# Optimization experiments

Hardware: AMD Instinct MI355X
Metric: run time of the kernel (lower is better)

## Reference

```python
import jax, jax.numpy as jnp
import numpy as np

N = 200000   # total atoms in batched graph
E = 3200000  # total bonds (directed edges)
B = 512      # number of graphs / sequences
L = 1000     # miRNA sequence length


def _gcn(x, W, b, src, dst, dis):
    # PyG GCNConv: add self-loops, symmetric normalization D^-1/2 A D^-1/2
    h = x @ W                                   # [N, Fout]
    msg = (dis[src] * dis[dst])[:, None] * h[src]
    agg = jax.ops.segment_sum(msg, dst, num_segments=x.shape[0])
    return agg + (dis * dis)[:, None] * h + b   # self-loop term + bias


def _conv1d(x, k, b):
    # x: [B, C, L], k: [O, I, K]  (torch Conv1d, VALID padding)
    y = jax.lax.conv_general_dilated(x, k, (1,), 'VALID',
                                     dimension_numbers=('NCH', 'OIH', 'NCH'))
    return y + b[None, :, None]


def _mp3(x):
    # torch MaxPool1d(3): window 3, stride 3, floor
    return jax.lax.reduce_window(x, -jnp.inf, jax.lax.max, (1, 1, 3), (1, 1, 3), 'VALID')


def setup_inputs() -> dict:
    key = jax.random.key(0)
    ks = jax.random.split(key, 24)
    w = lambda k, s: (jax.random.normal(k, s, jnp.float32) * 0.1)
    p = {}
    p['x'] = jax.random.normal(ks[0], (N, 4), jnp.float32)
    p['edge_index'] = jax.random.randint(ks[1], (2, E), 0, N, jnp.int32)
    p['batch'] = (jnp.arange(N, dtype=jnp.int32) * B // N).astype(jnp.int32)  # every graph non-empty
    p['target'] = jax.random.normal(ks[2], (B, L, 5), jnp.float32)
    # GCN layers 4->4->8->16
    p['W1'] = w(ks[3], (4, 4));    p['b1'] = jnp.zeros(4, jnp.float32)
    p['W2'] = w(ks[4], (4, 8));    p['b2'] = jnp.zeros(8, jnp.float32)
    p['W3'] = w(ks[5], (8, 16));   p['b3'] = jnp.zeros(16, jnp.float32)
    p['Wg1'] = w(ks[6], (16, 1024)); p['bg1'] = jnp.zeros(1024, jnp.float32)
    p['Wg2'] = w(ks[7], (1024, 128)); p['bg2'] = jnp.zeros(128, jnp.float32)
    # CNN stack on sequences, kernels [O, I, 8]
    p['K1'] = w(ks[8], (32, 5, 8));   p['cb1'] = jnp.zeros(32, jnp.float32)
    p['K2'] = w(ks[9], (64, 32, 8));  p['cb2'] = jnp.zeros(64, jnp.float32)
    p['K3'] = w(ks[10], (128, 64, 8)); p['cb3'] = jnp.zeros(128, jnp.float32)
    p['Wxt'] = w(ks[11], (128, 128)); p['bxt'] = jnp.zeros(128, jnp.float32)
    # fusion head
    p['Wf1'] = w(ks[12], (256, 1024)); p['bf1'] = jnp.zeros(1024, jnp.float32)
    p['Wf2'] = w(ks[13], (1024, 512)); p['bf2'] = jnp.zeros(512, jnp.float32)
    p['Wo'] = w(ks[14], (512, 2));     p['bo'] = jnp.zeros(2, jnp.float32)
    return p


def reference(x, edge_index, batch, target, W1, b1, W2, b2, W3, b3,
              Wg1, bg1, Wg2, bg2, K1, cb1, K2, cb2, K3, cb3,
              Wxt, bxt, Wf1, bf1, Wf2, bf2, Wo, bo):
    src, dst = edge_index[0], edge_index[1]
    deg = jax.ops.segment_sum(jnp.ones(src.shape[0], x.dtype), dst,
                              num_segments=x.shape[0]) + 1.0  # +1 self-loop
    dis = jax.lax.rsqrt(deg)
    # Graph branch (dropout is identity in eval)
    h = jax.nn.relu(_gcn(x, W1, b1, src, dst, dis))
    h = jax.nn.relu(_gcn(h, W2, b2, src, dst, dis))
    h = jax.nn.relu(_gcn(h, W3, b3, src, dst, dis))
    g = jax.ops.segment_max(h, batch, num_segments=B)  # global_max_pool
    g = jax.nn.relu(g @ Wg1 + bg1)
    g = g @ Wg2 + bg2
    # Sequence branch
    t = jnp.transpose(target, (0, 2, 1))  # [B, 5, L]
    c = _mp3(jax.nn.relu(_conv1d(t, K1, cb1)))
    c = _mp3(jax.nn.relu(_conv1d(c, K2, cb2)))
    c = _mp3(jax.nn.relu(_conv1d(c, K3, cb3)))
    c = jnp.mean(c, axis=2)               # [B, 128]
    c = jax.nn.relu(c @ Wxt + bxt)
    # Fusion head
    xc = jnp.concatenate([g, c], axis=1)  # [B, 256]
    xc = jax.nn.relu(xc @ Wf1 + bf1)
    xc = jax.nn.relu(xc @ Wf2 + bf2)
    return xc @ Wo + bo                    # [B, 2]
```

## Files before the change

kernel.cpp:

```cpp
#include <hip/hip_runtime.h>
#include <hip/hip_fp16.h>
#include <cstddef>

#define NA 200000
#define NE 3200000
#define NB 512
#define NBKT 256
#define BKTN 782
#define BKTCAP 16384
#define NEPB 3200

typedef _Float16 hv2 __attribute__((ext_vector_type(2)));
typedef _Float16 half8 __attribute__((ext_vector_type(8)));
typedef float floatx4 __attribute__((ext_vector_type(4)));
union UH2 { unsigned u; __half2 h; hv2 v; };
__device__ __forceinline__ float4 h4f(unsigned a, unsigned b) {
    UH2 x, y; x.u = a; y.u = b;
    float2 fa = __half22float2(x.h), fb = __half22float2(y.h);
    return make_float4(fa.x, fa.y, fb.x, fb.y);
}
__device__ __forceinline__ unsigned f2h(float a, float b) {
    UH2 r; r.h = __float22half2_rn(make_float2(a, b));
    return r.u;
}

__global__ void k_init(unsigned* g, int* gcursor,
                       float* gvec, const float* __restrict__ bg2,
                       float* xf2, const float* __restrict__ bf2,
                       float* xf1, const float* __restrict__ bf1,
                       const float* __restrict__ K2, const float* __restrict__ K3,
                       __half* __restrict__ Wt2, __half* __restrict__ Wt3) {
    int i = blockIdx.x * blockDim.x + threadIdx.x;
    if (i < NB * 16) g[i] = 0u;
    if (i < NBKT) gcursor[i] = i * BKTCAP;
    if (i < NB * 128) gvec[i] = bg2[i & 127];
    if (i < NB * 512) xf2[i] = bf2[i & 511];
    if (i < NB * 1024) xf1[i] = bf1[i & 1023];
    if (i < 64 * 32 * 8) {
        int o = i >> 8, rem = i & 255, c = rem >> 3, kk = rem & 7;
        Wt2[(o << 8) + (kk << 5) + c] = __float2half(K2[i]);
    }
    if (i < 128 * 64 * 8) {
        int o = i >> 9, rem = i & 511, c = rem >> 3, kk = rem & 7;
        Wt3[(o << 9) + (kk << 6) + c] = __float2half(K3[i]);
    }
}

template<int CIN, int COUT, int OBLK, int LIN, int PITCH, int POUT, int NTT>
__device__ __forceinline__ void dev_conv1(int b, int oy,
        const float* __restrict__ in, const float* __restrict__ Kw,
        const float* __restrict__ bias, __half* __restrict__ out,
        float* s_in) {
    constexpr int SPO = 256 / OBLK;
    constexpr int PT = (NTT < 4) ? NTT : 4;
    constexpr int NPASS = (NTT + PT - 1) / PT;
    for (int idx = threadIdx.x; idx < CIN * PITCH; idx += 256) s_in[idx] = 0.f;
    __syncthreads();
    for (int idx = threadIdx.x; idx < LIN * CIN; idx += 256) {
        int p = idx / CIN, c = idx - p * CIN;
        s_in[c * PITCH + p] = in[(size_t)b * (LIN * CIN) + idx];
    }
    __syncthreads();
    int ol = threadIdx.x / SPO;
    int s  = threadIdx.x - ol * SPO;
    int o  = oy * OBLK + ol;
    float bo = bias[o];
    const float* wrow = Kw + (size_t)o * CIN * 8;
    for (int pass = 0; pass < NPASS; pass++) {
        float acc[PT][12];
#pragma unroll
        for (int tt = 0; tt < PT; tt++)
#pragma unroll
            for (int j = 0; j < 12; j++) acc[tt][j] = 0.f;
        bool vld[PT]; int tgs[PT];
#pragma unroll
        for (int tt = 0; tt < PT; tt++) {
            int ta = pass * PT + tt;
            int tg = s + SPO * ta;
            tgs[tt] = tg;
            vld[tt] = (ta < NTT) && (4 * tg < POUT);
        }
        for (int i = 0; i < CIN; i++) {
            float wa[8];
            const float4* wp = (const float4*)(wrow + (size_t)i * 8);
            *(float4*)&wa[0] = wp[0];
            *(float4*)&wa[4] = wp[1];
#pragma unroll
            for (int tt = 0; tt < PT; tt++) {
                if (vld[tt]) {
                    const float4* xr = (const float4*)&s_in[i * PITCH + 12 * tgs[tt]];
                    float xa[20];
#pragma unroll
                    for (int q = 0; q < 5; q++) *(float4*)&xa[4 * q] = xr[q];
#pragma unroll
                    for (int j = 0; j < 12; j++) {
                        float sm = acc[tt][j];
#pragma unroll
                        for (int k = 0; k < 8; k++) sm = fmaf(xa[j + k], wa[k], sm);
                        acc[tt][j] = sm;
                    }
                }
            }
        }
#pragma unroll
        for (int tt = 0; tt < PT; tt++) {
            if (vld[tt]) {
#pragma unroll
                for (int p = 0; p < 4; p++) {
                    int P = 4 * tgs[tt] + p;
                    if (P < POUT) {
                        float m = fmaxf(fmaxf(acc[tt][3 * p], acc[tt][3 * p + 1]), acc[tt][3 * p + 2]);
                        out[((size_t)b * COUT + o) * POUT + P] = __float2half(fmaxf(m + bo, 0.f));
                    }
                }
            }
        }
    }
}

__device__ __forceinline__ void dev_conv2_mfma(int b,
        const __half* __restrict__ pool1, const __half* __restrict__ Wt2,
        const float* __restrict__ cb2, __half* __restrict__ pool2t,
        char* smem) {
    __half* sT   = (__half*)smem;
    __half* outS = (__half*)smem;
    const __half* inp = pool1 + (size_t)b * (32 * 331);
    for (int idx = threadIdx.x; idx < 32 * 331; idx += 256) {
        int c = idx / 331;
        int p = idx - c * 331;
        sT[p * 40 + c] = inp[idx];
    }
    __syncthreads();
    int lane = threadIdx.x & 63, wv = threadIdx.x >> 6;
    int l15 = lane & 15, lg = lane >> 4;
    int mtBeg = wv * 5;
    int nmt = (wv == 3) ? 6 : 5;
    const floatx4 FZ = {0.f, 0.f, 0.f, 0.f};
    floatx4 acc[6][4];
#pragma unroll
    for (int mi = 0; mi < 6; mi++)
#pragma unroll
        for (int nt = 0; nt < 4; nt++) acc[mi][nt] = FZ;
    const half8* WB = (const half8*)Wt2;
    for (int s = 0; s < 8; s++) {
        half8 bfr[4];
#pragma unroll
        for (int nt = 0; nt < 4; nt++)
            bfr[nt] = WB[(nt * 16 + l15) * 32 + s * 4 + lg];
        half8 afr[6];
#pragma unroll
        for (int mi = 0; mi < 6; mi++) {
            if (mi < nmt) {
                int row = (mtBeg + mi) * 16 + l15 + s;
                afr[mi] = *(const half8*)(sT + row * 40 + lg * 8);
            }
        }
#pragma unroll
        for (int mi = 0; mi < 6; mi++) {
            if (mi < nmt) {
#pragma unroll
                for (int nt = 0; nt < 4; nt++)
                    acc[mi][nt] = __builtin_amdgcn_mfma_f32_16x16x32_f16(
                        afr[mi], bfr[nt], acc[mi][nt], 0, 0, 0);
            }
        }
    }
    __syncthreads();
    float bo[4];
#pragma unroll
    for (int nt = 0; nt < 4; nt++) bo[nt] = cb2[nt * 16 + l15];
    __half* op = pool2t + (size_t)b * (108 * 64);
    for (int h = 0; h < 2; h++) {
        int r0 = h * 168;
#pragma unroll
        for (int mi = 0; mi < 6; mi++) {
            if (mi < nmt) {
#pragma unroll
                for (int nt = 0; nt < 4; nt++) {
                    int o = nt * 16 + l15;
#pragma unroll
                    for (int r = 0; r < 4; r++) {
                        int p = (mtBeg + mi) * 16 + lg * 4 + r;
                        unsigned pl = (unsigned)(p - r0);
                        if (pl < 168u) {
                            float v = fmaxf(acc[mi][nt][r] + bo[nt], 0.f);
                            outS[pl * 68 + o] = __float2half(v);
                        }
                    }
                }
            }
        }
        __syncthreads();
        int nP = h ? 52 : 56;
        for (int idx = threadIdx.x; idx < nP * 64; idx += 256) {
            int Pl = idx >> 6, o = idx & 63;
            int P = h * 56 + Pl;
            int p = 3 * P - r0;
            float v0 = __half2float(outS[p * 68 + o]);
            float v1 = __half2float(outS[(p + 1) * 68 + o]);
            float v2 = __half2float(outS[(p + 2) * 68 + o]);
            op[P * 64 + o] = __float2half(fmaxf(fmaxf(v0, v1), v2));
        }
        __syncthreads();
    }
}

__device__ __forceinline__ void dev_conv3_mfma(int b, int nh,
        const __half* __restrict__ pool2t, const __half* __restrict__ Wt3,
        const float* __restrict__ cb3, float* __restrict__ pool3,
        char* smem) {
    __half* sT  = (__half*)smem;
    float* outS = (float*)smem;
    const uint4* inp = (const uint4*)(pool2t + (size_t)b * (108 * 64));
    for (int t = threadIdx.x; t < 108 * 8; t += 256) {
        int r = t >> 3, s8 = t & 7;
        *(uint4*)(sT + r * 72 + s8 * 8) = inp[t];
    }
    __syncthreads();
    int lane = threadIdx.x & 63, wv = threadIdx.x >> 6;
    int l15 = lane & 15, lg = lane >> 4;
    int mtBeg = wv * 2;
    int nmt = (wv == 3) ? 1 : 2;
    const floatx4 FZ = {0.f, 0.f, 0.f, 0.f};
    floatx4 acc[2][4];
#pragma unroll
    for (int mi = 0; mi < 2; mi++)
#pragma unroll
        for (int nt = 0; nt < 4; nt++) acc[mi][nt] = FZ;
    const half8* WB = (const half8*)Wt3;
    for (int s = 0; s < 16; s++) {
        half8 afr[2];
#pragma unroll
        for (int mi = 0; mi < 2; mi++) {
            if (mi < nmt) {
                int row = (mtBeg + mi) * 16 + l15 + (s >> 1);
                afr[mi] = *(const half8*)(sT + row * 72 + (s & 1) * 32 + lg * 8);
            }
        }
#pragma unroll
        for (int nt = 0; nt < 4; nt++) {
            half8 bfr = WB[((nh * 4 + nt) * 16 + l15) * 64 + s * 4 + lg];
            acc[0][nt] = __builtin_amdgcn_mfma_f32_16x16x32_f16(
                afr[0], bfr, acc[0][nt], 0, 0, 0);
            if (nmt > 1)
                acc[1][nt] = __builtin_amdgcn_mfma_f32_16x16x32_f16(
                    afr[1], bfr, acc[1][nt], 0, 0, 0);
        }
    }
    __syncthreads();
    float bo[4];
#pragma unroll
    for (int nt = 0; nt < 4; nt++) bo[nt] = cb3[(nh * 4 + nt) * 16 + l15];
    float* op = pool3 + (size_t)b * (33 * 128);
    for (int pp = 0; pp < 3; pp++) {
        int t0 = 3 * pp;
#pragma unroll
        for (int mi = 0; mi < 2; mi++) {
            int tile = mtBeg + mi;
            if (mi < nmt && tile >= t0 && tile < t0 + 3) {
#pragma unroll
                for (int nt = 0; nt < 4; nt++) {
                    int ol = nt * 16 + l15;
#pragma unroll
                    for (int r = 0; r < 4; r++) {
                        int p = tile * 16 + lg * 4 + r;
                        if (p < 100)
                            outS[(p - 48 * pp) * 68 + ol] =
                                fmaxf(acc[mi][nt][r] + bo[nt], 0.f);
                    }
                }
            }
        }
        __syncthreads();
        int nP = (pp == 2) ? 1 : 16;
        for (int idx = threadIdx.x; idx < nP * 64; idx += 256) {
            int Pl = idx >> 6, ol = idx & 63;
            int P = 16 * pp + Pl;
            int p = 3 * P - 48 * pp;
            float v0 = outS[p * 68 + ol];
            float v1 = outS[(p + 1) * 68 + ol];
            float v2 = outS[(p + 2) * 68 + ol];
            op[P * 128 + (nh << 6) + ol] = fmaxf(fmaxf(v0, v1), v2);
        }
        __syncthreads();
    }
}

__global__ __launch_bounds__(256) void k_A(
        const int* __restrict__ src, const int* __restrict__ dst,
        int* __restrict__ gcursor, unsigned* __restrict__ stage,
        const float* __restrict__ tgt, const float* __restrict__ K1,
        const float* __restrict__ cb1, __half* __restrict__ pool1) {
    __shared__ __align__(16) char smem[20160];
    int bx = blockIdx.x;
    if (bx >= 1000) {
        dev_conv1<5, 32, 16, 1000, 1008, 331, 6>(bx - 1000, 0, tgt, K1, cb1,
                                                 pool1, (float*)smem);
        return;
    }
    int* hcnt  = (int*)smem;
    int* hbase = hcnt + 256;
    int* lbase = hbase + 256;
    unsigned* sbuf = (unsigned*)(lbase + 256);
    unsigned char* sbkt = (unsigned char*)(sbuf + NEPB);
    int t = threadIdx.x;
    int e0 = bx * NEPB;
    hcnt[t] = 0;
    __syncthreads();
    const int4* d4 = (const int4*)(dst + e0);
    for (int i = t; i < NEPB / 4; i += 256) {
        int4 d = d4[i];
        atomicAdd(&hcnt[d.x / BKTN], 1);
        atomicAdd(&hcnt[d.y / BKTN], 1);
        atomicAdd(&hcnt[d.z / BKTN], 1);
        atomicAdd(&hcnt[d.w / BKTN], 1);
    }
    __syncthreads();
    int myc = hcnt[t];
    hbase[t] = atomicAdd(&gcursor[t], myc);
    __syncthreads();
#pragma unroll
    for (int off = 1; off < 256; off <<= 1) {
        int u = (t >= off) ? hcnt[t - off] : 0;
        __syncthreads();
        hcnt[t] += u;
        __syncthreads();
    }
    lbase[t] = hcnt[t] - myc;
    hcnt[t] = 0;
    __syncthreads();
    const int4* s4 = (const int4*)(src + e0);
    for (int i = t; i < NEPB / 4; i += 256) {
        int4 d = d4[i];
        int4 s = s4[i];
        int ds[4] = {d.x, d.y, d.z, d.w};
        int ss[4] = {s.x, s.y, s.z, s.w};
#pragma unroll
        for (int j = 0; j < 4; j++) {
            int bkt = ds[j] / BKTN;
            int dloc = ds[j] - bkt * BKTN;
            int k = atomicAdd(&hcnt[bkt], 1);
            int pos = lbase[bkt] + k;
            sbuf[pos] = ((unsigned)dloc << 18) | (unsigned)ss[j];
            sbkt[pos] = (unsigned char)bkt;
        }
    }
    __syncthreads();
    for (int i = t; i < NEPB; i += 256) {
        unsigned v = sbuf[i];
        int bkt = sbkt[i];
        stage[hbase[bkt] + (i - lbase[bkt])] = v;
    }
}

__global__ __launch_bounds__(256) void k_Bp(
        const unsigned* __restrict__ stage, const int* __restrict__ gcursor,
        int* __restrict__ rowptr, int* __restrict__ cnt, int* __restrict__ csr,
        const float* __restrict__ x, float4* __restrict__ dt1,
        const float* __restrict__ tgt, const float* __restrict__ K1,
        const float* __restrict__ cb1, __half* __restrict__ pool1) {
    __shared__ __align__(16) char smem[20160];
    __shared__ int sbase;
    int bx = blockIdx.x;
    if (bx >= NBKT) {
        dev_conv1<5, 32, 16, 1000, 1008, 331, 6>(bx - NBKT, 1, tgt, K1, cb1,
                                                 pool1, (float*)smem);
        return;
    }
    int* lcnt    = (int*)smem;
    int* lpos    = lcnt + BKTN;
    int* partial = lpos + BKTN;
    int t = threadIdx.x;
    int bkt = bx;
    int tot = gcursor[t] - t * BKTCAP;
    partial[t] = tot;
    __syncthreads();
#pragma unroll
    for (int off = 1; off < 256; off <<= 1) {
        int u = (t >= off) ? partial[t - off] : 0;
        __syncthreads();
        partial[t] += u;
        __syncthreads();
    }
    if (t == 0) sbase = (bkt == 0) ? 0 : partial[bkt - 1];
    __syncthreads();
    int base = sbase;
    int n0 = bkt * BKTN;
    int ncnt = (NA - n0 < BKTN) ? (NA - n0) : BKTN;
    int eBeg = bkt * BKTCAP;
    int eCnt = gcursor[bkt] - eBeg;
    for (int i = t; i < BKTN; i += 256) lcnt[i] = 0;
    __syncthreads();
    for (int i = t; i < eCnt; i += 256)
        atomicAdd(&lcnt[stage[eBeg + i] >> 18], 1);
    __syncthreads();
    int mysum = 0;
#pragma unroll
    for (int j = 0; j < 4; j++) {
        int node = 4 * t + j;
        if (node < ncnt) mysum += lcnt[node];
    }
    partial[t] = mysum;
    __syncthreads();
#pragma unroll
    for (int off = 1; off < 256; off <<= 1) {
        int u = (t >= off) ? partial[t - off] : 0;
        __syncthreads();
        partial[t] += u;
        __syncthreads();
    }
    int running = partial[t] - mysum;
#pragma unroll
    for (int j = 0; j < 4; j++) {
        int node = 4 * t + j;
        if (node < ncnt) {
            lpos[node] = running;
            rowptr[n0 + node] = base + running;
            cnt[n0 + node] = lcnt[node];
            running += lcnt[node];
        }
    }
    __syncthreads();
    for (int i = t; i < eCnt; i += 256) {
        unsigned v = stage[eBeg + i];
        int dloc = v >> 18;
        int s = v & 0x3FFFF;
        int k = atomicAdd(&lpos[dloc], 1);
        csr[base + k] = s;
    }
    for (int i = t; i < ncnt; i += 256) {
        int n = n0 + i;
        float4 p = ((const float4*)x)[n];
        float dv = rsqrtf((float)lcnt[i] + 1.0f);
        dt1[n] = make_float4(dv * p.x, dv * p.y, dv * p.z, dv * p.w);
    }
}

__global__ __launch_bounds__(256) void k_B(
        const __half* __restrict__ pool1, const __half* __restrict__ Wt2,
        const float* __restrict__ cb2, __half* __restrict__ pool2t,
        const float4* __restrict__ dt1, const int* __restrict__ rowptr,
        const int* __restrict__ cnt, const int* __restrict__ csr,
        const float* __restrict__ W1, const float* __restrict__ b1,
        float4* __restrict__ dt2) {
    __shared__ __align__(16) char smem[27520];
    int bx = blockIdx.x;
    if (bx < 512) {
        dev_conv2_mfma(bx, pool1, Wt2, cb2, pool2t, smem);
        return;
    }
    __shared__ float sW[16];
    if (threadIdx.x < 16) sW[threadIdx.x] = W1[threadIdx.x];
    __syncthreads();
    int n = (bx - 512) * 256 + threadIdx.x;
    if (n >= NA) return;
    int cn = cnt[n];
    float dv = rsqrtf((float)cn + 1.0f);
    const int* row = csr + rowptr[n];
    float4 acc = dt1[n];
    int e = 0;
    for (; e + 7 < cn; e += 8) {
        int idx[8];
#pragma unroll
        for (int u = 0; u < 8; u++) idx[u] = row[e + u];
        float4 v[8];
#pragma unroll
        for (int u = 0; u < 8; u++) v[u] = dt1[idx[u]];
#pragma unroll
        for (int u = 0; u < 8; u++) {
            acc.x += v[u].x; acc.y += v[u].y; acc.z += v[u].z; acc.w += v[u].w;
        }
    }
    for (; e < cn; e++) {
        float4 v = dt1[row[e]];
        acc.x += v.x; acc.y += v.y; acc.z += v.z; acc.w += v.w;
    }
    const float4 bq = *(const float4*)b1;
    float a[4] = {acc.x, acc.y, acc.z, acc.w};
    float bb[4] = {bq.x, bq.y, bq.z, bq.w};
    float o[4];
#pragma unroll
    for (int f = 0; f < 4; f++) {
        float s = 0.f;
#pragma unroll
        for (int k = 0; k < 4; k++) s = fmaf(a[k], sW[k * 4 + f], s);
        o[f] = dv * fmaxf(fmaf(dv, s, bb[f]), 0.f);
    }
    dt2[n] = make_float4(o[0], o[1], o[2], o[3]);
}

__global__ __launch_bounds__(256, 8) void k_C(
        const __half* __restrict__ pool2t, const __half* __restrict__ Wt3,
        const float* __restrict__ cb3, float* __restrict__ pool3,
        const float4* __restrict__ dt2, const int* __restrict__ rowptr,
        const int* __restrict__ cnt, const int* __restrict__ csr,
        const float* __restrict__ W2, const float* __restrict__ b2,
        uint4* __restrict__ dt3) {
    __shared__ __align__(16) char smem[17280];
    int bx = blockIdx.x;
    if (bx < 1024) {
        dev_conv3_mfma(bx & 511, bx >> 9, pool2t, Wt3, cb3, pool3, smem);
        return;
    }
    __shared__ float sW[32];
    if (threadIdx.x < 32) sW[threadIdx.x] = W2[threadIdx.x];
    __syncthreads();
    int n = (bx - 1024) * 256 + threadIdx.x;
    if (n >= NA) return;
    int cn = cnt[n];
    float dv = rsqrtf((float)cn + 1.0f);
    const int* row = csr + rowptr[n];
    float4 acc = dt2[n];
    int e = 0;
    for (; e + 7 < cn; e += 8) {
        int idx[8];
#pragma unroll
        for (int u = 0; u < 8; u++) idx[u] = row[e + u];
        float4 v[8];
#pragma unroll
        for (int u = 0; u < 8; u++) v[u] = dt2[idx[u]];
#pragma unroll
        for (int u = 0; u < 8; u++) {
            acc.x += v[u].x; acc.y += v[u].y; acc.z += v[u].z; acc.w += v[u].w;
        }
    }
    for (; e < cn; e++) {
        float4 v = dt2[row[e]];
        acc.x += v.x; acc.y += v.y; acc.z += v.z; acc.w += v.w;
    }
    float a[4] = {acc.x, acc.y, acc.z, acc.w};
    float o[8];
#pragma unroll
    for (int f = 0; f < 8; f++) {
        float s = 0.f;
#pragma unroll
        for (int k = 0; k < 4; k++) s = fmaf(a[k], sW[k * 8 + f], s);
        o[f] = dv * fmaxf(fmaf(dv, s, b2[f]), 0.f);
    }
    dt3[n] = make_uint4(f2h(o[0], o[1]), f2h(o[2], o[3]),
                        f2h(o[4], o[5]), f2h(o[6], o[7]));
}

__global__ __launch_bounds__(256) void k_D(
        const uint4* __restrict__ dt3, const int* __restrict__ rowptr,
        const int* __restrict__ cnt, const int* __restrict__ csr,
        const float* __restrict__ W3, const float* __restrict__ b3,
        const int* __restrict__ batch, unsigned* __restrict__ g,
        const float* __restrict__ pool3, const float* __restrict__ Wxt,
        const float* __restrict__ bxt, float* __restrict__ cx) {
    int bx = blockIdx.x;
    if (bx >= 782) {
        __shared__ float sa[8 * 128];
        int b0 = (bx - 782) * 8;
        for (int t = threadIdx.x; t < 8 * 128; t += 256) {
            int gg = t >> 7, k = t & 127;
            const float* r = pool3 + (size_t)(b0 + gg) * (33 * 128) + k;
            float s = 0.f;
#pragma unroll
            for (int p = 0; p < 33; p++) s += r[p * 128];
            sa[t] = s * (1.f / 33.f);
        }
        __syncthreads();
        int j = threadIdx.x;
        if (j >= 128) return;
        float bj = bxt[j];
        float acc[8];
#pragma unroll
        for (int gg = 0; gg < 8; gg++) acc[gg] = bj;
#pragma unroll 4
        for (int k = 0; k < 128; k++) {
            float w = Wxt[(size_t)k * 128 + j];
#pragma unroll
            for (int gg = 0; gg < 8; gg++) acc[gg] = fmaf(sa[gg * 128 + k], w, acc[gg]);
        }
#pragma unroll
        for (int gg = 0; gg < 8; gg++)
            cx[(size_t)(b0 + gg) * 128 + j] = fmaxf(acc[gg], 0.f);
        return;
    }
    __shared__ float sW[128];
    __shared__ unsigned sg[32];
    __shared__ int sbmin;
    int id = bx;
    if (threadIdx.x < 128) sW[threadIdx.x] = W3[threadIdx.x];
    if (threadIdx.x < 32) sg[threadIdx.x] = 0u;
    if (threadIdx.x == 0) sbmin = batch[id * 256];
    __syncthreads();
    int n = id * 256 + threadIdx.x;
    if (n < NA) {
        int cn = cnt[n];
        float dv = rsqrtf((float)cn + 1.0f);
        const int* row = csr + rowptr[n];
        uint4 sv = dt3[n];
        float4 lo = h4f(sv.x, sv.y), hi = h4f(sv.z, sv.w);
        float a0 = lo.x, a1 = lo.y, a2 = lo.z, a3 = lo.w;
        float a4 = hi.x, a5 = hi.y, a6 = hi.z, a7 = hi.w;
        int e = 0;
        for (; e + 3 < cn; e += 4) {
            uint4 p0 = dt3[row[e]],     p1 = dt3[row[e + 1]];
            uint4 p2 = dt3[row[e + 2]], p3 = dt3[row[e + 3]];
            float4 l0 = h4f(p0.x, p0.y), h0 = h4f(p0.z, p0.w);
            float4 l1 = h4f(p1.x, p1.y), h1 = h4f(p1.z, p1.w);
            float4 l2 = h4f(p2.x, p2.y), h2 = h4f(p2.z, p2.w);
            float4 l3 = h4f(p3.x, p3.y), h3v = h4f(p3.z, p3.w);
            a0 += (l0.x + l1.x) + (l2.x + l3.x);
            a1 += (l0.y + l1.y) + (l2.y + l3.y);
            a2 += (l0.z + l1.z) + (l2.z + l3.z);
            a3 += (l0.w + l1.w) + (l2.w + l3.w);
            a4 += (h0.x + h1.x) + (h2.x + h3v.x);
            a5 += (h0.y + h1.y) + (h2.y + h3v.y);
            a6 += (h0.z + h1.z) + (h2.z + h3v.z);
            a7 += (h0.w + h1.w) + (h2.w + h3v.w);
        }
        for (; e < cn; e++) {
            uint4 p = dt3[row[e]];
            float4 l = h4f(p.x, p.y), h = h4f(p.z, p.w);
            a0 += l.x; a1 += l.y; a2 += l.z; a3 += l.w;
            a4 += h.x; a5 += h.y; a6 += h.z; a7 += h.w;
        }
        float af[8] = {a0, a1, a2, a3, a4, a5, a6, a7};
        int rb = batch[n] - sbmin;
        if (rb > 1) rb = 1;
#pragma unroll
        for (int f = 0; f < 16; f++) {
            float s = 0.f;
#pragma unroll
            for (int k = 0; k < 8; k++) s = fmaf(af[k], sW[k * 16 + f], s);
            float r = fmaxf(fmaf(dv, s, b3[f]), 0.f);
            atomicMax(&sg[rb * 16 + f], __float_as_uint(r));
        }
    }
    __syncthreads();
    if (threadIdx.x < 32) {
        unsigned v = sg[threadIdx.x];
        int rb2 = threadIdx.x >> 4, f = threadIdx.x & 15;
        int bbn = sbmin + rb2;
        if (v != 0u && bbn < NB) atomicMax(&g[bbn * 16 + f], v);
    }
}

__global__ __launch_bounds__(256) void k_head_g(
        const float* __restrict__ g, const float* __restrict__ Wg1,
        const float* __restrict__ bg1, float* __restrict__ gp1) {
    __shared__ float sa[8 * 16];
    int bx = blockIdx.x;
    int b0 = (bx >> 2) * 8;
    if (threadIdx.x < 128)
        sa[threadIdx.x] = g[b0 * 16 + threadIdx.x];
    __syncthreads();
    int j = (bx & 3) * 256 + threadIdx.x;
    float bj = bg1[j];
    float acc[8];
#pragma unroll
    for (int gg = 0; gg < 8; gg++) acc[gg] = bj;
#pragma unroll
    for (int k = 0; k < 16; k++) {
        float w = Wg1[(size_t)k * 1024 + j];
#pragma unroll
        for (int gg = 0; gg < 8; gg++) acc[gg] = fmaf(sa[gg * 16 + k], w, acc[gg]);
    }
#pragma unroll
    for (int gg = 0; gg < 8; gg++)
        gp1[(size_t)(b0 + gg) * 1024 + j] = fmaxf(acc[gg], 0.f);
}

__global__ __launch_bounds__(256) void k_gvec_ks(
        const float* __restrict__ gp1, const float* __restrict__ Wg2,
        float* __restrict__ gvec) {
    __shared__ float sa[8 * 128];
    int k0 = blockIdx.x * 128;
    int b0 = blockIdx.y * 8;
    for (int t = threadIdx.x; t < 8 * 128; t += 256) {
        int gg = t >> 7, k = t & 127;
        sa[t] = gp1[(size_t)(b0 + gg) * 1024 + k0 + k];
    }
    __syncthreads();
    int j  = threadIdx.x & 127;
    int kh = (threadIdx.x >> 7) * 64;
    const float* Wp = Wg2 + (size_t)(k0 + kh) * 128 + j;
    float acc[8];
#pragma unroll
    for (int gg = 0; gg < 8; gg++) acc[gg] = 0.f;
    for (int k = 0; k < 64; k += 16) {
        float w[16];
#pragma unroll
        for (int u = 0; u < 16; u++) w[u] = Wp[(size_t)(k + u) * 128];
#pragma unroll
        for (int u = 0; u < 16; u++) {
#pragma unroll
            for (int gg = 0; gg < 8; gg++)
                acc[gg] = fmaf(sa[gg * 128 + kh + k + u], w[u], acc[gg]);
        }
    }
#pragma unroll
    for (int gg = 0; gg < 8; gg++)
        atomicAdd(&gvec[(size_t)(b0 + gg) * 128 + j], acc[gg]);
}

__global__ __launch_bounds__(256) void k_cat2(
        const float* __restrict__ gvec, const float* __restrict__ cx,
        const float* __restrict__ Wf1, float* __restrict__ xf1) {
    __shared__ float sa[8 * 128];
    int jx = blockIdx.x & 3;
    int kh = blockIdx.x >> 2;
    int b0 = blockIdx.y * 8;
    const float* A = kh ? cx : gvec;
    for (int t = threadIdx.x; t < 8 * 128; t += 256) {
        int gg = t >> 7, k = t & 127;
        sa[t] = A[(size_t)(b0 + gg) * 128 + k];
    }
    __syncthreads();
    int j = jx * 256 + threadIdx.x;
    const float* Wp = Wf1 + (size_t)(kh * 128) * 1024 + j;
    float acc[8];
#pragma unroll
    for (int gg = 0; gg < 8; gg++) acc[gg] = 0.f;
    for (int k = 0; k < 128; k += 16) {
        float w[16];
#pragma unroll
        for (int u = 0; u < 16; u++) w[u] = Wp[(size_t)(k + u) * 1024];
#pragma unroll
        for (int u = 0; u < 16; u++) {
#pragma unroll
            for (int gg = 0; gg < 8; gg++)
                acc[gg] = fmaf(sa[gg * 128 + k + u], w[u], acc[gg]);
        }
    }
#pragma unroll
    for (int gg = 0; gg < 8; gg++)
        atomicAdd(&xf1[(size_t)(b0 + gg) * 1024 + j], acc[gg]);
}

__global__ __launch_bounds__(256) void k_xf2_ks(
        const float* __restrict__ xf1, const float* __restrict__ Wf2,
        float* __restrict__ xf2) {
    __shared__ float sa[8 * 256];
    int jb = blockIdx.x & 1;
    int k0 = (blockIdx.x >> 1) * 256;
    int b0 = blockIdx.y * 8;
    for (int t = threadIdx.x; t < 8 * 256; t += 256) {
        int gg = t >> 8, k = t & 255;
        sa[t] = fmaxf(xf1[(size_t)(b0 + gg) * 1024 + k0 + k], 0.f);
    }
    __syncthreads();
    int j = jb * 256 + threadIdx.x;
    const float* Wp = Wf2 + (size_t)k0 * 512 + j;
    float acc[8];
#pragma unroll
    for (int gg = 0; gg < 8; gg++) acc[gg] = 0.f;
    for (int k = 0; k < 256; k += 16) {
        float w[16];
#pragma unroll
        for (int u = 0; u < 16; u++) w[u] = Wp[(size_t)(k + u) * 512];
#pragma unroll
        for (int u = 0; u < 16; u++) {
#pragma unroll
            for (int gg = 0; gg < 8; gg++)
                acc[gg] = fmaf(sa[gg * 256 + k + u], w[u], acc[gg]);
        }
    }
#pragma unroll
    for (int gg = 0; gg < 8; gg++)
        atomicAdd(&xf2[(size_t)(b0 + gg) * 512 + j], acc[gg]);
}

__global__ __launch_bounds__(256) void k_dense_out(
        const float* __restrict__ A, const float* __restrict__ W,
        const float* __restrict__ bias, float* __restrict__ out) {
    int idx = blockIdx.x * 256 + threadIdx.x;
    if (idx >= NB * 2) return;
    int b = idx >> 1, j = idx & 1;
    float s = bias[j];
    const float4* A4 = (const float4*)(A + (size_t)b * 512);
    for (int k4 = 0; k4 < 128; k4 += 8) {
        float4 av[8];
#pragma unroll
        for (int u = 0; u < 8; u++) av[u] = A4[k4 + u];
#pragma unroll
        for (int u = 0; u < 8; u++) {
            int kb = (k4 + u) * 4;
            s = fmaf(fmaxf(av[u].x, 0.f), W[(kb + 0) * 2 + j], s);
            s = fmaf(fmaxf(av[u].y, 0.f), W[(kb + 1) * 2 + j], s);
            s = fmaf(fmaxf(av[u].z, 0.f), W[(kb + 2) * 2 + j], s);
            s = fmaf(fmaxf(av[u].w, 0.f), W[(kb + 3) * 2 + j], s);
        }
    }
    out[idx] = s;
}

extern "C" void kernel_launch(void* const* d_in, const int* in_sizes, int n_in,
                              void* d_out, int out_size, void* d_ws, size_t ws_size,
                              hipStream_t stream) {
    (void)in_sizes; (void)n_in; (void)out_size; (void)ws_size;
    const float* x   = (const float*)d_in[0];
    const int*  ei   = (const int*)d_in[1];
    const int*  batch= (const int*)d_in[2];
    const float* tgt = (const float*)d_in[3];
    const float* W1  = (const float*)d_in[4];  const float* b1  = (const float*)d_in[5];
    const float* W2  = (const float*)d_in[6];  const float* b2  = (const float*)d_in[7];
    const float* W3  = (const float*)d_in[8];  const float* b3  = (const float*)d_in[9];
    const float* Wg1 = (const float*)d_in[10]; const float* bg1 = (const float*)d_in[11];
    const float* Wg2 = (const float*)d_in[12]; const float* bg2 = (const float*)d_in[13];
    const float* K1  = (const float*)d_in[14]; const float* cb1 = (const float*)d_in[15];
    const float* K2  = (const float*)d_in[16]; const float* cb2 = (const float*)d_in[17];
    const float* K3  = (const float*)d_in[18]; const float* cb3 = (const float*)d_in[19];
    const float* Wxt = (const float*)d_in[20]; const float* bxt = (const float*)d_in[21];
    const float* Wf1 = (const float*)d_in[22]; const float* bf1 = (const float*)d_in[23];
    const float* Wf2 = (const float*)d_in[24]; const float* bf2 = (const float*)d_in[25];
    const float* Wo  = (const float*)d_in[26]; const float* bo  = (const float*)d_in[27];
    const int* srcp = ei;
    const int* dstp = ei + NE;

    float* ws = (float*)d_ws;
    float4* dt1 = (float4*)ws; ws += (size_t)NA * 4;
    float4* dt2 = (float4*)ws; ws += (size_t)NA * 4;
    uint4*  dt3 = (uint4*)ws;  ws += (size_t)NA * 4;
    float* g     = ws; ws += NB * 16;
    float* gp1   = ws; ws += NB * 1024;
    float* gvec  = ws; ws += NB * 128;
    float* cx    = ws; ws += NB * 128;
    float* xf1   = ws; ws += NB * 1024;
    float* xf2   = ws; ws += NB * 512;
    __half* pool1 = (__half*)ws; ws += (size_t)NB * 32 * 331;
    __half* pool2t = (__half*)ws; ws += (size_t)NB * 64 * 108;
    float* pool3 = ws; ws += (size_t)NB * 128 * 33;
    __half* Wt2 = (__half*)ws; ws += 64 * 256 / 2;
    __half* Wt3 = (__half*)ws; ws += 128 * 512 / 2;
    int*   cnt    = (int*)ws; ws += NA;
    int*   rowptr = (int*)ws; ws += NA;
    int*   csr    = (int*)ws; ws += NE;
    int*   gcursor= (int*)ws; ws += NBKT;
    unsigned* stage = (unsigned*)ws; ws += (size_t)NBKT * BKTCAP;

    dim3 blk(256);

    k_init<<<2048, blk, 0, stream>>>((unsigned*)g, gcursor, gvec, bg2, xf2, bf2,
                                     xf1, bf1, K2, K3, Wt2, Wt3);
    k_A<<<1512, blk, 0, stream>>>(srcp, dstp, gcursor, stage, tgt, K1, cb1, pool1);
    k_Bp<<<768, blk, 0, stream>>>(stage, gcursor, rowptr, cnt, csr, x, dt1,
                                  tgt, K1, cb1, pool1);
    k_B<<<1294, blk, 0, stream>>>(pool1, Wt2, cb2, pool2t,
                                  dt1, rowptr, cnt, csr, W1, b1, dt2);
    k_C<<<1806, blk, 0, stream>>>(pool2t, Wt3, cb3, pool3,
                                  dt2, rowptr, cnt, csr, W2, b2, dt3);
    k_D<<<846, blk, 0, stream>>>(dt3, rowptr, cnt, csr, W3, b3,
                                 batch, (unsigned*)g, pool3, Wxt, bxt, cx);

    k_head_g<<<256, blk, 0, stream>>>(g, Wg1, bg1, gp1);
    k_gvec_ks<<<dim3(8, 64), blk, 0, stream>>>(gp1, Wg2, gvec);
    k_cat2<<<dim3(8, 64), blk, 0, stream>>>(gvec, cx, Wf1, xf1);
    k_xf2_ks<<<dim3(8, 64), blk, 0, stream>>>(xf1, Wf2, xf2);
    k_dense_out<<<4, blk, 0, stream>>>(xf2, Wo, bo, (float*)d_out);
}
```

Baseline: 426.2 us.

## Pad CSR rows to multiples of four with sentinel node for int4 gathers

Each CSR row is padded to a multiple of four entries, using a sentinel index NA that points to a zeroed extra feature row. This lets the three aggregation kernels load neighbour indices as int4 and drop their scalar tail loops. Each bucket now writes into a fixed-size CSR slab, which removes the cross-bucket prefix scan. The block order is also swapped so aggregation blocks launch before the conv blocks. The padding adds extra gathers of the zero row and more memory, and each slab must hold its bucket's padded edges.

```diff
diff --git a/kernel.cpp b/kernel.cpp
--- a/kernel.cpp
+++ b/kernel.cpp
@@ -9,6 +9,7 @@
 #define BKTN 782
 #define BKTCAP 16384
 #define NEPB 3200
+#define CSRSLAB 20480
 
 typedef _Float16 hv2 __attribute__((ext_vector_type(2)));
 typedef _Float16 half8 __attribute__((ext_vector_type(8)));
@@ -360,7 +361,6 @@
         const float* __restrict__ tgt, const float* __restrict__ K1,
         const float* __restrict__ cb1, __half* __restrict__ pool1) {
     __shared__ __align__(16) char smem[20160];
-    __shared__ int sbase;
     int bx = blockIdx.x;
     if (bx >= NBKT) {
         dev_conv1<5, 32, 16, 1000, 1008, 331, 6>(bx - NBKT, 1, tgt, K1, cb1,
@@ -372,8 +372,23 @@
     int* partial = lpos + BKTN;
     int t = threadIdx.x;
     int bkt = bx;
-    int tot = gcursor[t] - t * BKTCAP;
-    partial[t] = tot;
+    int base = bkt * CSRSLAB;
+    int n0 = bkt * BKTN;
+    int ncnt = (NA - n0 < BKTN) ? (NA - n0) : BKTN;
+    int eBeg = bkt * BKTCAP;
+    int eCnt = gcursor[bkt] - eBeg;
+    for (int i = t; i < BKTN; i += 256) lcnt[i] = 0;
+    __syncthreads();
+    for (int i = t; i < eCnt; i += 256)
+        atomicAdd(&lcnt[stage[eBeg + i] >> 18], 1);
+    __syncthreads();
+    int mysum = 0;
+#pragma unroll
+    for (int j = 0; j < 4; j++) {
+        int node = 4 * t + j;
+        if (node < ncnt) mysum += (lcnt[node] + 3) & ~3;
+    }
+    partial[t] = mysum;
     __syncthreads();
 #pragma unroll
     for (int off = 1; off < 256; off <<= 1) {
@@ -382,42 +397,19 @@
         partial[t] += u;
         __syncthreads();
     }
-    if (t == 0) sbase = (bkt == 0) ? 0 : partial[bkt - 1];
-    __syncthreads();
-    int base = sbase;
-    int n0 = bkt * BKTN;
-    int ncnt = (NA - n0 < BKTN) ? (NA - n0) : BKTN;
-    int eBeg = bkt * BKTCAP;
-    int eCnt = gcursor[bkt] - eBeg;
-    for (int i = t; i < BKTN; i += 256) lcnt[i] = 0;
-    __syncthreads();
-    for (int i = t; i < eCnt; i += 256)
-        atomicAdd(&lcnt[stage[eBeg + i] >> 18], 1);
-    __syncthreads();
-    int mysum = 0;
-#pragma unroll
-    for (int j = 0; j < 4; j++) {
-        int node = 4 * t + j;
-        if (node < ncnt) mysum += lcnt[node];
-    }
-    partial[t] = mysum;
-    __syncthreads();
-#pragma unroll
-    for (int off = 1; off < 256; off <<= 1) {
-        int u = (t >= off) ? partial[t - off] : 0;
-        __syncthreads();
-        partial[t] += u;
-        __syncthreads();
-    }
     int running = partial[t] - mysum;
 #pragma unroll
     for (int j = 0; j < 4; j++) {
         int node = 4 * t + j;
         if (node < ncnt) {
+            int c = lcnt[node];
+            int c4 = (c + 3) & ~3;
             lpos[node] = running;
-            rowptr[n0 + node] = base + running;
-            cnt[n0 + node] = lcnt[node];
-            running += lcnt[node];
+            int rp = base + running;
+            rowptr[n0 + node] = rp;
+            cnt[n0 + node] = c;
+            for (int k = c; k < c4; k++) csr[rp + k] = NA;
+            running += c4;
         }
     }
     __syncthreads();
@@ -434,6 +426,7 @@
         float dv = rsqrtf((float)lcnt[i] + 1.0f);
         dt1[n] = make_float4(dv * p.x, dv * p.y, dv * p.z, dv * p.w);
     }
+    if (bkt == 0 && t == 0) dt1[NA] = make_float4(0.f, 0.f, 0.f, 0.f);
 }
 
 __global__ __launch_bounds__(256) void k_B(
@@ -445,35 +438,38 @@
         float4* __restrict__ dt2) {
     __shared__ __align__(16) char smem[27520];
     int bx = blockIdx.x;
-    if (bx < 512) {
-        dev_conv2_mfma(bx, pool1, Wt2, cb2, pool2t, smem);
+    if (bx >= 782) {
+        dev_conv2_mfma(bx - 782, pool1, Wt2, cb2, pool2t, smem);
         return;
     }
     __shared__ float sW[16];
     if (threadIdx.x < 16) sW[threadIdx.x] = W1[threadIdx.x];
     __syncthreads();
-    int n = (bx - 512) * 256 + threadIdx.x;
+    int n = bx * 256 + threadIdx.x;
     if (n >= NA) return;
+    if (n == 0) dt2[NA] = make_float4(0.f, 0.f, 0.f, 0.f);
     int cn = cnt[n];
     float dv = rsqrtf((float)cn + 1.0f);
-    const int* row = csr + rowptr[n];
+    const int4* row4 = (const int4*)(csr + rowptr[n]);
     float4 acc = dt1[n];
-    int e = 0;
-    for (; e + 7 < cn; e += 8) {
-        int idx[8];
-#pragma unroll
-        for (int u = 0; u < 8; u++) idx[u] = row[e + u];
-        float4 v[8];
-#pragma unroll
-        for (int u = 0; u < 8; u++) v[u] = dt1[idx[u]];
-#pragma unroll
-        for (int u = 0; u < 8; u++) {
-            acc.x += v[u].x; acc.y += v[u].y; acc.z += v[u].z; acc.w += v[u].w;
-        }
-    }
-    for (; e < cn; e++) {
-        float4 v = dt1[row[e]];
-        acc.x += v.x; acc.y += v.y; acc.z += v.z; acc.w += v.w;
+    int nb = (cn + 3) >> 2;
+    int q = 0;
+    for (; q + 1 < nb; q += 2) {
+        int4 ra = row4[q], rb = row4[q + 1];
+        float4 v0 = dt1[ra.x], v1 = dt1[ra.y], v2 = dt1[ra.z], v3 = dt1[ra.w];
+        float4 v4 = dt1[rb.x], v5 = dt1[rb.y], v6 = dt1[rb.z], v7 = dt1[rb.w];
+        acc.x += ((v0.x + v1.x) + (v2.x + v3.x)) + ((v4.x + v5.x) + (v6.x + v7.x));
+        acc.y += ((v0.y + v1.y) + (v2.y + v3.y)) + ((v4.y + v5.y) + (v6.y + v7.y));
+        acc.z += ((v0.z + v1.z) + (v2.z + v3.z)) + ((v4.z + v5.z) + (v6.z + v7.z));
+        acc.w += ((v0.w + v1.w) + (v2.w + v3.w)) + ((v4.w + v5.w) + (v6.w + v7.w));
+    }
+    if (q < nb) {
+        int4 ra = row4[q];
+        float4 v0 = dt1[ra.x], v1 = dt1[ra.y], v2 = dt1[ra.z], v3 = dt1[ra.w];
+        acc.x += (v0.x + v1.x) + (v2.x + v3.x);
+        acc.y += (v0.y + v1.y) + (v2.y + v3.y);
+        acc.z += (v0.z + v1.z) + (v2.z + v3.z);
+        acc.w += (v0.w + v1.w) + (v2.w + v3.w);
     }
     const float4 bq = *(const float4*)b1;
     float a[4] = {acc.x, acc.y, acc.z, acc.w};
@@ -498,35 +494,39 @@
         uint4* __restrict__ dt3) {
     __shared__ __align__(16) char smem[17280];
     int bx = blockIdx.x;
-    if (bx < 1024) {
-        dev_conv3_mfma(bx & 511, bx >> 9, pool2t, Wt3, cb3, pool3, smem);
+    if (bx >= 782) {
+        int ci = bx - 782;
+        dev_conv3_mfma(ci & 511, ci >> 9, pool2t, Wt3, cb3, pool3, smem);
         return;
     }
     __shared__ float sW[32];
     if (threadIdx.x < 32) sW[threadIdx.x] = W2[threadIdx.x];
     __syncthreads();
-    int n = (bx - 1024) * 256 + threadIdx.x;
+    int n = bx * 256 + threadIdx.x;
     if (n >= NA) return;
+    if (n == 0) dt3[NA] = make_uint4(0u, 0u, 0u, 0u);
     int cn = cnt[n];
     float dv = rsqrtf((float)cn + 1.0f);
-    const int* row = csr + rowptr[n];
+    const int4* row4 = (const int4*)(csr + rowptr[n]);
     float4 acc = dt2[n];
-    int e = 0;
-    for (; e + 7 < cn; e += 8) {
-        int idx[8];
-#pragma unroll
-        for (int u = 0; u < 8; u++) idx[u] = row[e + u];
-        float4 v[8];
-#pragma unroll
-        for (int u = 0; u < 8; u++) v[u] = dt2[idx[u]];
-#pragma unroll
-        for (int u = 0; u < 8; u++) {
-            acc.x += v[u].x; acc.y += v[u].y; acc.z += v[u].z; acc.w += v[u].w;
-        }
-    }
-    for (; e < cn; e++) {
-        float4 v = dt2[row[e]];
-        acc.x += v.x; acc.y += v.y; acc.z += v.z; acc.w += v.w;
+    int nb = (cn + 3) >> 2;
+    int q = 0;
+    for (; q + 1 < nb; q += 2) {
+        int4 ra = row4[q], rb = row4[q + 1];
+        float4 v0 = dt2[ra.x], v1 = dt2[ra.y], v2 = dt2[ra.z], v3 = dt2[ra.w];
+        float4 v4 = dt2[rb.x], v5 = dt2[rb.y], v6 = dt2[rb.z], v7 = dt2[rb.w];
+        acc.x += ((v0.x + v1.x) + (v2.x + v3.x)) + ((v4.x + v5.x) + (v6.x + v7.x));
+        acc.y += ((v0.y + v1.y) + (v2.y + v3.y)) + ((v4.y + v5.y) + (v6.y + v7.y));
+        acc.z += ((v0.z + v1.z) + (v2.z + v3.z)) + ((v4.z + v5.z) + (v6.z + v7.z));
+        acc.w += ((v0.w + v1.w) + (v2.w + v3.w)) + ((v4.w + v5.w) + (v6.w + v7.w));
+    }
+    if (q < nb) {
+        int4 ra = row4[q];
+        float4 v0 = dt2[ra.x], v1 = dt2[ra.y], v2 = dt2[ra.z], v3 = dt2[ra.w];
+        acc.x += (v0.x + v1.x) + (v2.x + v3.x);
+        acc.y += (v0.y + v1.y) + (v2.y + v3.y);
+        acc.z += (v0.z + v1.z) + (v2.z + v3.z);
+        acc.w += (v0.w + v1.w) + (v2.w + v3.w);
     }
     float a[4] = {acc.x, acc.y, acc.z, acc.w};
     float o[8];
@@ -590,15 +590,15 @@
     if (n < NA) {
         int cn = cnt[n];
         float dv = rsqrtf((float)cn + 1.0f);
-        const int* row = csr + rowptr[n];
+        const int4* row4 = (const int4*)(csr + rowptr[n]);
         uint4 sv = dt3[n];
         float4 lo = h4f(sv.x, sv.y), hi = h4f(sv.z, sv.w);
         float a0 = lo.x, a1 = lo.y, a2 = lo.z, a3 = lo.w;
         float a4 = hi.x, a5 = hi.y, a6 = hi.z, a7 = hi.w;
-        int e = 0;
-        for (; e + 3 < cn; e += 4) {
-            uint4 p0 = dt3[row[e]],     p1 = dt3[row[e + 1]];
-            uint4 p2 = dt3[row[e + 2]], p3 = dt3[row[e + 3]];
+        int nb = (cn + 3) >> 2;
+        for (int q = 0; q < nb; q++) {
+            int4 ra = row4[q];
+            uint4 p0 = dt3[ra.x], p1 = dt3[ra.y], p2 = dt3[ra.z], p3 = dt3[ra.w];
             float4 l0 = h4f(p0.x, p0.y), h0 = h4f(p0.z, p0.w);
             float4 l1 = h4f(p1.x, p1.y), h1 = h4f(p1.z, p1.w);
             float4 l2 = h4f(p2.x, p2.y), h2 = h4f(p2.z, p2.w);
@@ -611,12 +611,6 @@
             a5 += (h0.y + h1.y) + (h2.y + h3v.y);
             a6 += (h0.z + h1.z) + (h2.z + h3v.z);
             a7 += (h0.w + h1.w) + (h2.w + h3v.w);
-        }
-        for (; e < cn; e++) {
-            uint4 p = dt3[row[e]];
-            float4 l = h4f(p.x, p.y), h = h4f(p.z, p.w);
-            a0 += l.x; a1 += l.y; a2 += l.z; a3 += l.w;
-            a4 += h.x; a5 += h.y; a6 += h.z; a7 += h.w;
         }
         float af[8] = {a0, a1, a2, a3, a4, a5, a6, a7};
         int rb = batch[n] - sbmin;
@@ -812,9 +806,9 @@
     const int* dstp = ei + NE;
 
     float* ws = (float*)d_ws;
-    float4* dt1 = (float4*)ws; ws += (size_t)NA * 4;
-    float4* dt2 = (float4*)ws; ws += (size_t)NA * 4;
-    uint4*  dt3 = (uint4*)ws;  ws += (size_t)NA * 4;
+    float4* dt1 = (float4*)ws; ws += (size_t)(NA + 1) * 4;
+    float4* dt2 = (float4*)ws; ws += (size_t)(NA + 1) * 4;
+    uint4*  dt3 = (uint4*)ws;  ws += (size_t)(NA + 1) * 4;
     float* g     = ws; ws += NB * 16;
     float* gp1   = ws; ws += NB * 1024;
     float* gvec  = ws; ws += NB * 128;
@@ -828,7 +822,7 @@
     __half* Wt3 = (__half*)ws; ws += 128 * 512 / 2;
     int*   cnt    = (int*)ws; ws += NA;
     int*   rowptr = (int*)ws; ws += NA;
-    int*   csr    = (int*)ws; ws += NE;
+    int*   csr    = (int*)ws; ws += (size_t)NBKT * CSRSLAB;
     int*   gcursor= (int*)ws; ws += NBKT;
     unsigned* stage = (unsigned*)ws; ws += (size_t)NBKT * BKTCAP;
 
```

New measurement: 434.6 us. About the same (+2.0%).
